# Kernel tuning notes

Hardware: AMD Instinct MI355X
Metric: run time of the kernel (lower is better)

## Reference

```python
import jax, jax.numpy as jnp
import numpy as np

B, N, D = 2, 2048, 1024
H = 16
DH = D // H
WINDOW = 64
SCALE = 1.0 / np.sqrt(DH).astype(np.float32)


def setup_inputs() -> dict:
    key = jax.random.key(0)
    k1, k2, k3 = jax.random.split(key, 3)
    # xavier-uniform-like scales for the projections
    lim_qkv = np.sqrt(6.0 / (D + 3 * D)).astype(np.float32)
    lim_out = np.sqrt(6.0 / (D + D)).astype(np.float32)
    x = jax.random.normal(k1, (B, N, D), dtype=jnp.float32)
    Wqkv = jax.random.uniform(k2, (3 * D, D), dtype=jnp.float32, minval=-lim_qkv, maxval=lim_qkv)
    bqkv = jnp.zeros((3 * D,), dtype=jnp.float32)
    Wout = jax.random.uniform(k3, (D, D), dtype=jnp.float32, minval=-lim_out, maxval=lim_out)
    bout = jnp.zeros((D,), dtype=jnp.float32)
    return {"x": x, "Wqkv": Wqkv, "bqkv": bqkv, "Wout": Wout, "bout": bout}


def _causal_window_mask(n: int) -> jnp.ndarray:
    pos = jnp.arange(n)
    diff = pos[:, None] - pos[None, :]  # query_pos - key_pos
    return (diff >= 0) & (diff < WINDOW)  # [N, N] bool


def reference(x, Wqkv, bqkv, Wout, bout):
    b, n, d = x.shape
    qkv = x @ Wqkv.T + bqkv                      # [B, N, 3D]
    qkv = qkv.reshape(b, n, 3, H, DH)
    qkv = jnp.transpose(qkv, (2, 0, 3, 1, 4))    # [3, B, H, N, DH]
    q, k, v = qkv[0], qkv[1], qkv[2]
    scores = jnp.einsum('bhqd,bhkd->bhqk', q, k) * SCALE  # [B, H, N, N]
    mask = _causal_window_mask(n)
    neg_inf = jnp.asarray(-jnp.inf, dtype=scores.dtype)
    scores = jnp.where(mask[None, None], scores, neg_inf)
    attn = jax.nn.softmax(scores, axis=-1)
    out = jnp.einsum('bhqk,bhkd->bhqd', attn, v)  # [B, H, N, DH]
    out = jnp.transpose(out, (0, 2, 1, 3)).reshape(b, n, d)
    return out @ Wout.T + bout
```

## Files before the change

kernel.cpp:

```cpp
#include <hip/hip_runtime.h>
#include <hip/hip_bf16.h>


typedef __attribute__((ext_vector_type(8))) __bf16 bf16x8;
typedef __attribute__((ext_vector_type(4))) float f32x4;

#define GLOAD16(g, l)                                              \
  __builtin_amdgcn_global_load_lds(                                \
      (const __attribute__((address_space(1))) void*)(g),          \
      (__attribute__((address_space(3))) void*)(l), 16, 0, 0)

#define MFMA16(a, b, c) __builtin_amdgcn_mfma_f32_16x16x32_bf16((a), (b), (c), 0, 0, 0)

__global__ __launch_bounds__(256) void cvt3(const float* __restrict__ x,
                                            const float* __restrict__ wqkv,
                                            const float* __restrict__ wout,
                                            __bf16* __restrict__ xb,
                                            __bf16* __restrict__ wqkvb,
                                            __bf16* __restrict__ woutb) {
  const int blk = blockIdx.x;
  const float* src;
  __bf16* dst;
  int i;
  if (blk < 2048) {
    src = x; dst = xb; i = (blk * 256 + (int)threadIdx.x) * 8;
  } else if (blk < 3584) {
    src = wqkv; dst = wqkvb; i = ((blk - 2048) * 256 + (int)threadIdx.x) * 8;
  } else {
    src = wout; dst = woutb; i = ((blk - 3584) * 256 + (int)threadIdx.x) * 8;
  }
  f32x4 a = *(const f32x4*)(src + i);
  f32x4 b = *(const f32x4*)(src + i + 4);
  bf16x8 o;
  o[0] = (__bf16)a[0]; o[1] = (__bf16)a[1]; o[2] = (__bf16)a[2]; o[3] = (__bf16)a[3];
  o[4] = (__bf16)b[0]; o[5] = (__bf16)b[1]; o[6] = (__bf16)b[2]; o[7] = (__bf16)b[3];
  *(bf16x8*)(dst + i) = o;
}

template <int MODE>
__global__ __launch_bounds__(256) void gemm128(
    const __bf16* __restrict__ A, const __bf16* __restrict__ Bw,
    const float* __restrict__ bias, int M, int N, int K,
    float* __restrict__ outF,
    __bf16* __restrict__ qo, __bf16* __restrict__ ko, __bf16* __restrict__ vt) {
  __shared__ __align__(16) unsigned char As[128 * 256];
  __shared__ __align__(16) unsigned char Bs[128 * 256];
  const int tid = threadIdx.x;
  const int lane = tid & 63;
  const int wid = tid >> 6;
  const int wr = wid >> 1, wc = wid & 1;
  const int colL = lane & 15, g = lane >> 4;
  const int m0 = blockIdx.x * 128, n0 = blockIdx.y * 128;

  f32x4 acc[4][4] = {};

  const int nK = K >> 7;
  for (int ks = 0; ks < nK; ++ks) {
    const int k0 = ks << 7;
    __syncthreads();
#pragma unroll
    for (int it = 0; it < 8; ++it) {
      int c = tid + (it << 8);
      int row = c >> 4, p = c & 15;
      int q = p ^ (row & 7);
      GLOAD16(A + (size_t)(m0 + row) * K + (k0 + (q << 3)), As + c * 16);
      GLOAD16(Bw + (size_t)(n0 + row) * K + (k0 + (q << 3)), Bs + c * 16);
    }
    __syncthreads();
#pragma unroll
    for (int kk = 0; kk < 4; ++kk) {
      bf16x8 af[4], bf[4];
      const int slot = (kk << 2) + g;
#pragma unroll
      for (int mi = 0; mi < 4; ++mi) {
        int r = (wr << 6) + (mi << 4) + colL;
        af[mi] = *(const bf16x8*)(As + r * 256 + ((slot ^ (r & 7)) << 4));
      }
#pragma unroll
      for (int ni = 0; ni < 4; ++ni) {
        int r = (wc << 6) + (ni << 4) + colL;
        bf[ni] = *(const bf16x8*)(Bs + r * 256 + ((slot ^ (r & 7)) << 4));
      }
#pragma unroll
      for (int mi = 0; mi < 4; ++mi)
#pragma unroll
        for (int ni = 0; ni < 4; ++ni)
          acc[mi][ni] = MFMA16(af[mi], bf[ni], acc[mi][ni]);
    }
  }

#pragma unroll
  for (int ni = 0; ni < 4; ++ni) {
    const int Cn = n0 + (wc << 6) + (ni << 4) + colL;
    const float bv = bias[Cn];
    if (MODE == 0) {
      const int sx = Cn >> 10, h = (Cn >> 6) & 15, d = Cn & 63;
      const float mul = (sx == 0) ? 0.125f : 1.0f;
#pragma unroll
      for (int mi = 0; mi < 4; ++mi) {
#pragma unroll
        for (int j = 0; j < 4; ++j) {
          const int Rm = m0 + (wr << 6) + (mi << 4) + (g << 2) + j;
          const int bb = Rm >> 11, tt = Rm & 2047;
          const float v = (acc[mi][ni][j] + bv) * mul;
          if (sx == 2) {
            vt[(((size_t)bb * 16 + h) * 64 + d) * 2048 + tt] = (__bf16)v;
          } else {
            __bf16* dst = (sx == 0) ? qo : ko;
            dst[(((size_t)bb * 16 + h) * 2048 + tt) * 64 + d] = (__bf16)v;
          }
        }
      }
    } else {
#pragma unroll
      for (int mi = 0; mi < 4; ++mi) {
#pragma unroll
        for (int j = 0; j < 4; ++j) {
          const int Rm = m0 + (wr << 6) + (mi << 4) + (g << 2) + j;
          outF[(size_t)Rm * N + Cn] = acc[mi][ni][j] + bv;
        }
      }
    }
  }
}

__global__ __launch_bounds__(256) void attn_win(const __bf16* __restrict__ Qb,
                                                const __bf16* __restrict__ Kb,
                                                const __bf16* __restrict__ Vt,
                                                __bf16* __restrict__ Ob) {
  const int bh = blockIdx.x >> 5;
  const int qb = blockIdx.x & 31;
  const int b = bh >> 4, h = bh & 15;
  __shared__ __align__(16) unsigned char Qs[64 * 128];
  __shared__ __align__(16) unsigned char Ks[128 * 128];
  __shared__ __align__(16) unsigned char Vs[64 * 256];
  __shared__ __align__(16) unsigned char Ps[4 * 16 * 272];
  const int tid = threadIdx.x;
  const int lane = tid & 63;
  const int w = tid >> 6;
  const int colL = lane & 15, g = lane >> 4;
  const __bf16* Qg = Qb + (size_t)bh * 2048 * 64;
  const __bf16* Kg = Kb + (size_t)bh * 2048 * 64;
  const __bf16* Vg = Vt + (size_t)bh * 64 * 2048;
  const int t0 = qb * 64 - 64;

#pragma unroll
  for (int it = 0; it < 2; ++it) {
    int c = tid + (it << 8);
    int r = c >> 3, p = c & 7, q = p ^ (r & 7);
    GLOAD16(Qg + (size_t)(qb * 64 + r) * 64 + (q << 3), Qs + c * 16);
  }
#pragma unroll
  for (int it = 0; it < 4; ++it) {
    int c = tid + (it << 8);
    int r = c >> 3, p = c & 7, q = p ^ (r & 7);
    int tok = t0 + r;
    tok = tok < 0 ? 0 : tok;
    GLOAD16(Kg + (size_t)tok * 64 + (q << 3), Ks + c * 16);
  }
#pragma unroll
  for (int it = 0; it < 4; ++it) {
    int c = tid + (it << 8);
    int r = c >> 4, p = c & 15, q = p ^ (r & 7);
    int tk = t0 + (q << 3);
    tk = tk < 0 ? 0 : tk;
    GLOAD16(Vg + (size_t)r * 2048 + tk, Vs + c * 16);
  }
  __syncthreads();

  f32x4 sc[8] = {};
  bf16x8 qf[2];
#pragma unroll
  for (int kk = 0; kk < 2; ++kk) {
    int r = (w << 4) + colL;
    int slot = (kk << 2) + g;
    qf[kk] = *(const bf16x8*)(Qs + r * 128 + ((slot ^ (r & 7)) << 4));
  }
#pragma unroll
  for (int ni = 0; ni < 8; ++ni) {
#pragma unroll
    for (int kk = 0; kk < 2; ++kk) {
      int r = (ni << 4) + colL;
      int slot = (kk << 2) + g;
      bf16x8 kf = *(const bf16x8*)(Ks + r * 128 + ((slot ^ (r & 7)) << 4));
      sc[ni] = MFMA16(qf[kk], kf, sc[ni]);
    }
  }

  float mx[4], sm[4];
#pragma unroll
  for (int j = 0; j < 4; ++j) mx[j] = -3.0e38f;
#pragma unroll
  for (int ni = 0; ni < 8; ++ni) {
#pragma unroll
    for (int j = 0; j < 4; ++j) {
      const int qi = (w << 4) + (g << 2) + j;
      const int ki = (ni << 4) + colL;
      const bool valid = (ki > qi) && (ki <= qi + 64) && (qb > 0 || ki >= 64);
      if (!valid) sc[ni][j] = -3.0e38f;
      mx[j] = fmaxf(mx[j], sc[ni][j]);
    }
  }
#pragma unroll
  for (int j = 0; j < 4; ++j) {
    mx[j] = fmaxf(mx[j], __shfl_xor(mx[j], 1));
    mx[j] = fmaxf(mx[j], __shfl_xor(mx[j], 2));
    mx[j] = fmaxf(mx[j], __shfl_xor(mx[j], 4));
    mx[j] = fmaxf(mx[j], __shfl_xor(mx[j], 8));
    sm[j] = 0.0f;
  }
  unsigned char* ps = Ps + w * (16 * 272);
#pragma unroll
  for (int ni = 0; ni < 8; ++ni) {
#pragma unroll
    for (int j = 0; j < 4; ++j) {
      float p = __expf(sc[ni][j] - mx[j]);
      sm[j] += p;
      *(__bf16*)(ps + ((g << 2) + j) * 272 + (((ni << 4) + colL) << 1)) = (__bf16)p;
    }
  }
#pragma unroll
  for (int j = 0; j < 4; ++j) {
    sm[j] += __shfl_xor(sm[j], 1);
    sm[j] += __shfl_xor(sm[j], 2);
    sm[j] += __shfl_xor(sm[j], 4);
    sm[j] += __shfl_xor(sm[j], 8);
  }
  __syncthreads();

  f32x4 o[4] = {};
#pragma unroll
  for (int step = 0; step < 4; ++step) {
    bf16x8 pf = *(const bf16x8*)(ps + colL * 272 + (step << 6) + (g << 4));
#pragma unroll
    for (int dt = 0; dt < 4; ++dt) {
      int r = (dt << 4) + colL;
      int slot = (step << 2) + g;
      bf16x8 vf = *(const bf16x8*)(Vs + r * 256 + ((slot ^ (r & 7)) << 4));
      o[dt] = MFMA16(pf, vf, o[dt]);
    }
  }

  float rinv[4];
#pragma unroll
  for (int j = 0; j < 4; ++j) rinv[j] = 1.0f / sm[j];
#pragma unroll
  for (int dt = 0; dt < 4; ++dt) {
#pragma unroll
    for (int j = 0; j < 4; ++j) {
      const int t = qb * 64 + (w << 4) + (g << 2) + j;
      Ob[((size_t)b * 2048 + t) * 1024 + h * 64 + (dt << 4) + colL] =
          (__bf16)(o[dt][j] * rinv[j]);
    }
  }
}

extern "C" void kernel_launch(void* const* d_in, const int* in_sizes, int n_in,
                              void* d_out, int out_size, void* d_ws, size_t ws_size,
                              hipStream_t stream) {
  const float* x = (const float*)d_in[0];
  const float* Wqkv = (const float*)d_in[1];
  const float* bqkv = (const float*)d_in[2];
  const float* Wout = (const float*)d_in[3];
  const float* bout = (const float*)d_in[4];
  float* out = (float*)d_out;

  __bf16* xb = (__bf16*)d_ws;
  __bf16* Wqkvb = xb + 4194304;
  __bf16* Woutb = Wqkvb + 3145728;
  __bf16* Qb = Woutb + 1048576;
  __bf16* Kb = Qb + 4194304;
  __bf16* Vtb = Kb + 4194304;
  __bf16* AOb = Vtb + 4194304;

  cvt3<<<4096, 256, 0, stream>>>(x, Wqkv, Wout, xb, Wqkvb, Woutb);
  gemm128<0><<<dim3(32, 24), 256, 0, stream>>>(xb, Wqkvb, bqkv, 4096, 3072, 1024,
                                               nullptr, Qb, Kb, Vtb);
  attn_win<<<1024, 256, 0, stream>>>(Qb, Kb, Vtb, AOb);
  gemm128<1><<<dim3(32, 8), 256, 0, stream>>>(AOb, Woutb, bout, 4096, 1024, 1024,
                                              out, nullptr, nullptr, nullptr);
}
```

Baseline: 86.99 us.

## Replace GEMMs with single-wave 64x64 tiles, double-buffered K loop, XCD-aware mapping

Both projection GEMMs now use one wave per 64x64 tile with a K step of 32, double-buffered async global-to-LDS loads, and waitcnt-based pipelining in place of block-wide barriers. Block indices are remapped so each XCD works on a contiguous region of M and N, aiming for better L2 reuse. The V-transposed output is staged through LDS so global writes are coalesced along the token dimension. The grid grows to 3072 and 1024 small blocks, which adds occupancy and overlap but reuses each loaded tile less.

Result: slower. 96.43 us (+10.9%).

```diff
diff --git a/kernel.cpp b/kernel.cpp
--- a/kernel.cpp
+++ b/kernel.cpp
@@ -37,88 +37,139 @@
   *(bf16x8*)(dst + i) = o;
 }
 
-template <int MODE>
-__global__ __launch_bounds__(256) void gemm128(
+template <int MODE, int RN>
+__global__ __launch_bounds__(64) void gemm_sw(
     const __bf16* __restrict__ A, const __bf16* __restrict__ Bw,
-    const float* __restrict__ bias, int M, int N, int K,
+    const float* __restrict__ bias,
     float* __restrict__ outF,
     __bf16* __restrict__ qo, __bf16* __restrict__ ko, __bf16* __restrict__ vt) {
-  __shared__ __align__(16) unsigned char As[128 * 256];
-  __shared__ __align__(16) unsigned char Bs[128 * 256];
-  const int tid = threadIdx.x;
-  const int lane = tid & 63;
-  const int wid = tid >> 6;
-  const int wr = wid >> 1, wc = wid & 1;
+  constexpr int K = 1024;
+  __shared__ __align__(16) unsigned char Ls[16384];
+  const int lane = (int)threadIdx.x;
   const int colL = lane & 15, g = lane >> 4;
-  const int m0 = blockIdx.x * 128, n0 = blockIdx.y * 128;
+
+  const int xcd = (int)blockIdx.x & 7;
+  const int i = (int)blockIdx.x >> 3;
+  const int mR = (xcd >> 1) * 16 + i / RN;
+  const int nR = (xcd & 1) * RN + i % RN;
+  const int m0 = mR * 64, n0 = nR * 64;
+
+  const __bf16* Ap = A + (size_t)m0 * K;
+  const __bf16* Bp = Bw + (size_t)n0 * K;
+
+  auto stg = [&](const __bf16* src, unsigned char* lds, int k0) {
+#pragma unroll
+    for (int it = 0; it < 4; ++it) {
+      int c = lane + (it << 6);
+      int L = c >> 3, s6 = c & 7;
+      int u = s6 ^ (L & 7);
+      int row = (L << 1) | (u >> 2), p = u & 3;
+      GLOAD16(src + (size_t)row * K + k0 + (p << 3), lds + c * 16);
+    }
+  };
 
   f32x4 acc[4][4] = {};
 
-  const int nK = K >> 7;
-  for (int ks = 0; ks < nK; ++ks) {
-    const int k0 = ks << 7;
-    __syncthreads();
-#pragma unroll
-    for (int it = 0; it < 8; ++it) {
-      int c = tid + (it << 8);
-      int row = c >> 4, p = c & 15;
-      int q = p ^ (row & 7);
-      GLOAD16(A + (size_t)(m0 + row) * K + (k0 + (q << 3)), As + c * 16);
-      GLOAD16(Bw + (size_t)(n0 + row) * K + (k0 + (q << 3)), Bs + c * 16);
-    }
-    __syncthreads();
-#pragma unroll
-    for (int kk = 0; kk < 4; ++kk) {
-      bf16x8 af[4], bf[4];
-      const int slot = (kk << 2) + g;
+  stg(Ap, Ls, 0);
+  stg(Bp, Ls + 4096, 0);
+  stg(Ap, Ls + 8192, 32);
+  stg(Bp, Ls + 12288, 32);
+  asm volatile("s_waitcnt vmcnt(8)" ::: "memory");
+
+  for (int t = 0; t < 32; ++t) {
+    const unsigned char* Ab = Ls + (t & 1) * 8192;
+    const unsigned char* Bb = Ab + 4096;
+    bf16x8 af[4], bf[4];
+#pragma unroll
+    for (int mi = 0; mi < 4; ++mi) {
+      const int r = (mi << 4) + colL;
+      af[mi] = *(const bf16x8*)(Ab + (r >> 1) * 128 +
+                                (((((r & 1) << 2) | g) ^ ((r >> 1) & 7)) << 4));
+    }
+#pragma unroll
+    for (int ni = 0; ni < 4; ++ni) {
+      const int r = (ni << 4) + colL;
+      bf[ni] = *(const bf16x8*)(Bb + (r >> 1) * 128 +
+                                (((((r & 1) << 2) | g) ^ ((r >> 1) & 7)) << 4));
+    }
+#pragma unroll
+    for (int mi = 0; mi < 4; ++mi)
+#pragma unroll
+      for (int ni = 0; ni < 4; ++ni)
+        acc[mi][ni] = MFMA16(af[mi], bf[ni], acc[mi][ni]);
+    if (t < 30) {
+      asm volatile("s_waitcnt lgkmcnt(0)" ::: "memory");
+      __builtin_amdgcn_sched_barrier(0);
+      unsigned char* d = Ls + (t & 1) * 8192;
+      const int kn = (t + 2) << 5;
+      stg(Ap, d, kn);
+      stg(Bp, d + 4096, kn);
+      asm volatile("s_waitcnt vmcnt(8)" ::: "memory");
+    } else if (t == 30) {
+      asm volatile("s_waitcnt vmcnt(0)" ::: "memory");
+    }
+  }
+
+  if (MODE == 0) {
+    const int sx = n0 >> 10, h = (n0 >> 6) & 15;
+    float bv[4];
+#pragma unroll
+    for (int ni = 0; ni < 4; ++ni) bv[ni] = bias[n0 + (ni << 4) + colL];
+    const int b = m0 >> 11, tt0 = m0 & 2047;
+    if (sx == 2) {
+      unsigned char* wreg = Ls;
+#pragma unroll
+      for (int mi = 0; mi < 4; ++mi)
+#pragma unroll
+        for (int ni = 0; ni < 4; ++ni)
+#pragma unroll
+          for (int jp = 0; jp < 2; ++jp) {
+            const int tt = (mi << 4) + (g << 2) + (jp << 1);
+            const int d = (ni << 4) + colL;
+            unsigned short u0 = __builtin_bit_cast(
+                unsigned short, (__bf16)(acc[mi][ni][jp * 2] + bv[ni]));
+            unsigned short u1 = __builtin_bit_cast(
+                unsigned short, (__bf16)(acc[mi][ni][jp * 2 + 1] + bv[ni]));
+            *(unsigned int*)(wreg + ((d * 72 + tt) << 1)) =
+                (unsigned int)u0 | ((unsigned int)u1 << 16);
+          }
+      asm volatile("s_waitcnt lgkmcnt(0)" ::: "memory");
+      const size_t vbase = (size_t)(b * 16 + h) * 64 * 2048;
+#pragma unroll
+      for (int i2 = 0; i2 < 32; ++i2) {
+        const int d = (i2 << 1) + (lane >> 5);
+        const int toff = (lane & 31) << 1;
+        unsigned int v = *(unsigned int*)(wreg + (d * 144 + ((lane & 31) << 2)));
+        *(unsigned int*)((unsigned short*)vt + vbase + (size_t)d * 2048 + tt0 + toff) = v;
+      }
+    } else {
+      __bf16* dst = (sx == 0) ? qo : ko;
+      const float mul = (sx == 0) ? 0.125f : 1.0f;
 #pragma unroll
       for (int mi = 0; mi < 4; ++mi) {
-        int r = (wr << 6) + (mi << 4) + colL;
-        af[mi] = *(const bf16x8*)(As + r * 256 + ((slot ^ (r & 7)) << 4));
-      }
-#pragma unroll
-      for (int ni = 0; ni < 4; ++ni) {
-        int r = (wc << 6) + (ni << 4) + colL;
-        bf[ni] = *(const bf16x8*)(Bs + r * 256 + ((slot ^ (r & 7)) << 4));
-      }
-#pragma unroll
-      for (int mi = 0; mi < 4; ++mi)
-#pragma unroll
-        for (int ni = 0; ni < 4; ++ni)
-          acc[mi][ni] = MFMA16(af[mi], bf[ni], acc[mi][ni]);
-    }
-  }
-
-#pragma unroll
-  for (int ni = 0; ni < 4; ++ni) {
-    const int Cn = n0 + (wc << 6) + (ni << 4) + colL;
-    const float bv = bias[Cn];
-    if (MODE == 0) {
-      const int sx = Cn >> 10, h = (Cn >> 6) & 15, d = Cn & 63;
-      const float mul = (sx == 0) ? 0.125f : 1.0f;
-#pragma unroll
-      for (int mi = 0; mi < 4; ++mi) {
 #pragma unroll
         for (int j = 0; j < 4; ++j) {
-          const int Rm = m0 + (wr << 6) + (mi << 4) + (g << 2) + j;
-          const int bb = Rm >> 11, tt = Rm & 2047;
-          const float v = (acc[mi][ni][j] + bv) * mul;
-          if (sx == 2) {
-            vt[(((size_t)bb * 16 + h) * 64 + d) * 2048 + tt] = (__bf16)v;
-          } else {
-            __bf16* dst = (sx == 0) ? qo : ko;
-            dst[(((size_t)bb * 16 + h) * 2048 + tt) * 64 + d] = (__bf16)v;
-          }
+          const int tt = tt0 + (mi << 4) + (g << 2) + j;
+          __bf16* rowp = dst + (((size_t)b * 16 + h) * 2048 + tt) * 64;
+#pragma unroll
+          for (int ni = 0; ni < 4; ++ni)
+            rowp[(ni << 4) + colL] = (__bf16)((acc[mi][ni][j] + bv[ni]) * mul);
         }
       }
-    } else {
-#pragma unroll
-      for (int mi = 0; mi < 4; ++mi) {
-#pragma unroll
-        for (int j = 0; j < 4; ++j) {
-          const int Rm = m0 + (wr << 6) + (mi << 4) + (g << 2) + j;
-          outF[(size_t)Rm * N + Cn] = acc[mi][ni][j] + bv;
-        }
+    }
+  } else {
+    float bv[4];
+#pragma unroll
+    for (int ni = 0; ni < 4; ++ni) bv[ni] = bias[n0 + (ni << 4) + colL];
+#pragma unroll
+    for (int mi = 0; mi < 4; ++mi) {
+#pragma unroll
+      for (int j = 0; j < 4; ++j) {
+        const int Rm = m0 + (mi << 4) + (g << 2) + j;
+        float* rowp = outF + (size_t)Rm * 1024 + n0;
+#pragma unroll
+        for (int ni = 0; ni < 4; ++ni)
+          rowp[(ni << 4) + colL] = acc[mi][ni][j] + bv[ni];
       }
     }
   }
@@ -274,9 +325,8 @@
   __bf16* AOb = Vtb + 4194304;
 
   cvt3<<<4096, 256, 0, stream>>>(x, Wqkv, Wout, xb, Wqkvb, Woutb);
-  gemm128<0><<<dim3(32, 24), 256, 0, stream>>>(xb, Wqkvb, bqkv, 4096, 3072, 1024,
-                                               nullptr, Qb, Kb, Vtb);
+  gemm_sw<0, 24><<<3072, 64, 0, stream>>>(xb, Wqkvb, bqkv, nullptr, Qb, Kb, Vtb);
   attn_win<<<1024, 256, 0, stream>>>(Qb, Kb, Vtb, AOb);
-  gemm128<1><<<dim3(32, 8), 256, 0, stream>>>(AOb, Woutb, bout, 4096, 1024, 1024,
-                                              out, nullptr, nullptr, nullptr);
+  gemm_sw<1, 8><<<1024, 64, 0, stream>>>(AOb, Woutb, bout, out,
+                                         nullptr, nullptr, nullptr);
 }
```
